# Performance work log

Measured on AMD Instinct MI355X. Metric: run time of the kernel, lower is better.

Reference implementation:

```python
import jax, jax.numpy as jnp
import numpy as np

K = 7  # g_decode_kernel_size


def _linear(x, W, b):
    # torch nn.Linear: y = x @ W.T + b, W: [out, in]
    return jnp.matmul(x, W.T) + b


def _shifted_conv(x, w, b):
    # x: [B, D, L]; causal conv: pad left K-1 (== pad both sides K-1 then trim right K-1)
    y = jax.lax.conv_general_dilated(
        x, w, window_strides=(1,), padding=[(K - 1, 0)],
        dimension_numbers=("NCH", "OIH", "NCH"))
    y = y + b[None, :, None]  # [B, 2D, L]
    D = x.shape[1]
    gated = y[:, :D, :] * jax.nn.sigmoid(y[:, D:, :])
    return gated + x


def setup_inputs() -> dict:
    key = jax.random.key(0)
    ks = jax.random.split(key, 16)
    B, T, L = 64, 64, 32
    E_enc, emb, D, A, V = 1024, 512, 512, 512, 30000

    def rn(k, shape, fan_in):
        return jax.random.normal(k, shape, dtype=jnp.float32) * (1.0 / np.sqrt(fan_in))

    return {
        "features": jax.random.normal(ks[0], (B, T, E_enc), dtype=jnp.float32),
        "captions": jax.random.randint(ks[1], (B, L), 0, V),
        "lengths": jax.random.randint(ks[2], (B,), 0, L),
        "embed_W": jax.random.normal(ks[3], (V, emb), dtype=jnp.float32) * 0.02,
        "W1": rn(ks[4], (D, emb + E_enc), emb + E_enc),
        "b1": jnp.zeros((D,), jnp.float32),
        "conv_w1": rn(ks[5], (2 * D, D, K), D * K),
        "conv_b1": jnp.zeros((2 * D,), jnp.float32),
        "conv_w2": rn(ks[6], (2 * D, D, K), D * K),
        "conv_b2": jnp.zeros((2 * D,), jnp.float32),
        "Wenc": rn(ks[7], (A, E_enc), E_enc),
        "benc": jnp.zeros((A,), jnp.float32),
        "Wdec": rn(ks[8], (A, D), D),
        "bdec": jnp.zeros((A,), jnp.float32),
        "Wp": rn(ks[9], (1, A), A),
        "bp": jnp.zeros((1,), jnp.float32),
        "W2": rn(ks[10], (V, E_enc + D), E_enc + D),
        "b2": jnp.zeros((V,), jnp.float32),
    }


def reference(features, captions, lengths, embed_W, W1, b1, conv_w1, conv_b1,
              conv_w2, conv_b2, Wenc, benc, Wdec, bdec, Wp, bp, W2, b2):
    # features: [B, T, E_enc]; captions: [B, L] int
    embeddings = embed_W[captions]                      # [B, L, emb]
    enc_mean = jnp.mean(features, axis=1, keepdims=True)  # [B, 1, E_enc]
    enc_mean = jnp.broadcast_to(enc_mean, (features.shape[0], embeddings.shape[1], features.shape[2]))
    x = jnp.concatenate([enc_mean, embeddings], axis=2)  # [B, L, E_enc+emb]
    x = _linear(x, W1, b1)                               # [B, L, D]
    x = jnp.transpose(x, (0, 2, 1))                      # [B, D, L]
    x = _shifted_conv(x, conv_w1, conv_b1)
    x = _shifted_conv(x, conv_w2, conv_b2)
    decode = jnp.transpose(x, (0, 2, 1))[:, :-1, :]      # [B, L-1, D]

    # Attention (vectorized over decode steps). NOTE: original code computes
    # tanh but discards it (assigns to misspelled 'featrues'), so NO tanh here.
    f_att = _linear(features, Wenc, benc)                # [B, T, A]
    d_att = _linear(decode, Wdec, bdec)                  # [B, S, A]
    # linear_prob applied to (f_att[:,None,t]+d_att[:,s,None]) -> scalar scores
    scores = (f_att[:, None, :, :] + d_att[:, :, None, :]) @ Wp[0] + bp[0]  # [B, S, T]
    attw = jax.nn.softmax(scores, axis=-1)               # softmax over T
    ctx = jnp.einsum("bst,bte->bse", attw, features)     # [B, S, E_enc]

    out = jnp.concatenate([ctx, decode], axis=2)         # [B, S, E_enc+D]
    logits = _linear(out, W2, b2)                        # [B, S, vocab]
    return logits
```

## Files before the change

### kernel.cpp

```cpp
#include <hip/hip_runtime.h>
#include <hip/hip_bf16.h>
#include <math.h>

#define B 64
#define T 64
#define E_ENC 1024
#define EMB 512
#define D 512
#define L 32
#define S 31
#define A 512
#define V 30000
#define KSZ 7
#define KC (D * KSZ)

typedef __attribute__((ext_vector_type(8))) short bf16x8;
typedef __attribute__((ext_vector_type(4))) float f32x4;

__device__ __forceinline__ unsigned short f2bf(float f) {
  union { float f; unsigned int u; } x; x.f = f;
  unsigned int r = (x.u + 0x7fffu + ((x.u >> 16) & 1u)) >> 16;
  return (unsigned short)r;
}

__device__ __forceinline__ void gload_lds16(const void* g, void* l) {
  __builtin_amdgcn_global_load_lds(
      (const __attribute__((address_space(1))) unsigned int*)g,
      (__attribute__((address_space(3))) unsigned int*)l, 16, 0, 0);
}

__global__ void k_wv(const float* __restrict__ Wenc, const float* __restrict__ Wp,
                     const float* __restrict__ benc, float* __restrict__ wv,
                     float* __restrict__ c0) {
  __shared__ float red[256];
  int e = blockIdx.x * 256 + threadIdx.x;
  float s = 0.f;
  for (int a = 0; a < A; ++a) s += Wp[a] * Wenc[(size_t)a * E_ENC + e];
  wv[e] = s;
  if (blockIdx.x == 0) {
    int t = threadIdx.x;
    float v = Wp[t] * benc[t] + Wp[t + 256] * benc[t + 256];
    red[t] = v;
    __syncthreads();
    for (int off = 128; off > 0; off >>= 1) {
      if (t < off) red[t] += red[t + off];
      __syncthreads();
    }
    if (t == 0) c0[0] = red[0];
  }
}

__global__ void k_mean_ctx(const float* __restrict__ features, const float* __restrict__ wv,
                           const float* __restrict__ c0, unsigned short* __restrict__ enc_meanb,
                           unsigned short* __restrict__ ctxb) {
  int b = blockIdx.x, tid = threadIdx.x;
  const float* fb = features + (size_t)b * T * E_ENC;
  __shared__ float s_attw[T];

  float m0 = 0, m1 = 0, m2 = 0, m3 = 0;
  for (int t = 0; t < T; ++t) {
    const float* r = fb + t * E_ENC;
    m0 += r[tid]; m1 += r[tid + 256]; m2 += r[tid + 512]; m3 += r[tid + 768];
  }
  size_t eb = (size_t)b * E_ENC;
  enc_meanb[eb + tid]       = f2bf(m0 * (1.f / 64.f));
  enc_meanb[eb + tid + 256] = f2bf(m1 * (1.f / 64.f));
  enc_meanb[eb + tid + 512] = f2bf(m2 * (1.f / 64.f));
  enc_meanb[eb + tid + 768] = f2bf(m3 * (1.f / 64.f));

  {
    int t = tid >> 2, part = tid & 3;
    const float* r = fb + t * E_ENC + part * 256;
    const float* wp = wv + part * 256;
    float s = 0.f;
    for (int e = 0; e < 256; e += 4) {
      float4 f4 = *(const float4*)(r + e);
      float4 w4 = *(const float4*)(wp + e);
      s += f4.x * w4.x + f4.y * w4.y + f4.z * w4.z + f4.w * w4.w;
    }
    s += __shfl_xor(s, 1);
    s += __shfl_xor(s, 2);
    if (part == 0) s_attw[t] = s + c0[0];
  }
  __syncthreads();
  if (tid < 64) {
    float v = s_attw[tid];
    float mx = v;
    #pragma unroll
    for (int off = 32; off > 0; off >>= 1) mx = fmaxf(mx, __shfl_xor(mx, off));
    float e = expf(v - mx);
    float sm = e;
    #pragma unroll
    for (int off = 32; off > 0; off >>= 1) sm += __shfl_xor(sm, off);
    s_attw[tid] = e / sm;
  }
  __syncthreads();
  float ca = 0, cb = 0, cc = 0, cd = 0;
  for (int t = 0; t < T; ++t) {
    float w = s_attw[t];
    const float* r = fb + t * E_ENC;
    ca += w * r[tid]; cb += w * r[tid + 256]; cc += w * r[tid + 512]; cd += w * r[tid + 768];
  }
  ctxb[eb + tid]       = f2bf(ca);
  ctxb[eb + tid + 256] = f2bf(cb);
  ctxb[eb + tid + 512] = f2bf(cc);
  ctxb[eb + tid + 768] = f2bf(cd);
}

__global__ void k_gather_emb(const float* __restrict__ embed_W,
                             const int* __restrict__ captions,
                             unsigned short* __restrict__ Xe) {
  int g = blockIdx.x, tid = threadIdx.x;
  int cap = captions[g];
  const float* src = embed_W + (size_t)cap * EMB;
  float2 v = *(const float2*)(src + tid * 2);
  unsigned int pk = (unsigned int)f2bf(v.x) | ((unsigned int)f2bf(v.y) << 16);
  *(unsigned int*)(Xe + (size_t)g * EMB + tid * 2) = pk;
}

__global__ void k_cvt_w1(const float* __restrict__ W1, unsigned short* __restrict__ w1b) {
  int d = blockIdx.x, tid = threadIdx.x;
  #pragma unroll
  for (int i = 0; i < 3; ++i) {
    int c = tid * 2 + i * 512;
    float2 v = *(const float2*)(W1 + (size_t)d * (E_ENC + EMB) + c);
    unsigned int pk = (unsigned int)f2bf(v.x) | ((unsigned int)f2bf(v.y) << 16);
    *(unsigned int*)(w1b + (size_t)d * (E_ENC + EMB) + c) = pk;
  }
}

__global__ __launch_bounds__(256) void k_x1f_mfma(
    const unsigned short* __restrict__ enc_meanb,
    const unsigned short* __restrict__ Xe,
    const unsigned short* __restrict__ w1b,
    const float* __restrict__ b1, float* __restrict__ x1) {
  __shared__ __align__(16) unsigned short As[64 * 64];
  __shared__ __align__(16) unsigned short Bs[64 * 64];
  int c0 = blockIdx.x * 64, g0 = blockIdx.y * 64;
  int tid = threadIdx.x, lane = tid & 63, wave = tid >> 6;
  int wr = wave >> 1, wc = wave & 1;
  int rsel = lane & 15, hi = lane >> 4;

  f32x4 acc[2][2];
  #pragma unroll
  for (int m = 0; m < 2; ++m)
    #pragma unroll
    for (int n = 0; n < 2; ++n) acc[m][n] = (f32x4){0.f, 0.f, 0.f, 0.f};

  int r1 = tid >> 3, s1 = tid & 7;
  int sw = (s1 ^ (r1 & 7)) * 8;
  const unsigned short* emA1 = enc_meanb + (size_t)(g0 >> 5) * 1024 + sw;
  const unsigned short* emA2 = enc_meanb + (size_t)((g0 >> 5) + 1) * 1024 + sw;
  const unsigned short* xeA1 = Xe + (size_t)(g0 + r1) * 512 + sw;
  const unsigned short* xeA2 = Xe + (size_t)(g0 + r1 + 32) * 512 + sw;
  const unsigned short* gB1 = w1b + (size_t)(c0 + r1) * (E_ENC + EMB) + sw;
  const unsigned short* gB2 = w1b + (size_t)(c0 + r1 + 32) * (E_ENC + EMB) + sw;
  unsigned short* aD1 = As + wave * 512;
  unsigned short* aD2 = As + 2048 + wave * 512;
  unsigned short* bD1 = Bs + wave * 512;
  unsigned short* bD2 = Bs + 2048 + wave * 512;

  int slot0 = hi ^ (rsel & 7);
  int slot1 = (4 + hi) ^ (rsel & 7);

  for (int kt = 0; kt < 24; ++kt) {
    const unsigned short *pA1, *pA2;
    if (kt < 16) { pA1 = emA1 + kt * 64; pA2 = emA2 + kt * 64; }
    else         { pA1 = xeA1 + (kt - 16) * 64; pA2 = xeA2 + (kt - 16) * 64; }
    gload_lds16(pA1, aD1);
    gload_lds16(pA2, aD2);
    gload_lds16(gB1, bD1);
    gload_lds16(gB2, bD2);
    gB1 += 64; gB2 += 64;
    __syncthreads();

    bf16x8 af[2][2], bfr[2][2];
    #pragma unroll
    for (int m = 0; m < 2; ++m) {
      int rowA = (wr * 32 + m * 16 + rsel) * 64;
      af[m][0] = *(const bf16x8*)(As + rowA + slot0 * 8);
      af[m][1] = *(const bf16x8*)(As + rowA + slot1 * 8);
    }
    #pragma unroll
    for (int n = 0; n < 2; ++n) {
      int rowB = (wc * 32 + n * 16 + rsel) * 64;
      bfr[n][0] = *(const bf16x8*)(Bs + rowB + slot0 * 8);
      bfr[n][1] = *(const bf16x8*)(Bs + rowB + slot1 * 8);
    }
    #pragma unroll
    for (int m = 0; m < 2; ++m)
      #pragma unroll
      for (int n = 0; n < 2; ++n) {
        acc[m][n] = __builtin_amdgcn_mfma_f32_16x16x32_bf16(af[m][0], bfr[n][0], acc[m][n], 0, 0, 0);
        acc[m][n] = __builtin_amdgcn_mfma_f32_16x16x32_bf16(af[m][1], bfr[n][1], acc[m][n], 0, 0, 0);
      }
    __syncthreads();
  }

  float bvv[2];
  #pragma unroll
  for (int n = 0; n < 2; ++n) bvv[n] = b1[c0 + wc * 32 + n * 16 + rsel];
  #pragma unroll
  for (int m = 0; m < 2; ++m)
    #pragma unroll
    for (int i = 0; i < 4; ++i) {
      int g = g0 + wr * 32 + m * 16 + hi * 4 + i;
      float* xr = x1 + (size_t)g * D;
      #pragma unroll
      for (int n = 0; n < 2; ++n) {
        int c = c0 + wc * 32 + n * 16 + rsel;
        xr[c] = acc[m][n][i] + bvv[n];
      }
    }
}

__global__ void k_im2col(const float* __restrict__ x, unsigned short* __restrict__ Xc) {
  int g = blockIdx.x, tid = threadIdx.x;
  int b = g >> 5, l = g & 31;
  unsigned short* row = Xc + (size_t)g * KC;
  const float* xb = x + (size_t)b * L * D;
  int d = tid * 2;
  #pragma unroll
  for (int k = 0; k < KSZ; ++k) {
    int lp = l + k - 6;
    unsigned int pk = 0;
    if (lp >= 0) {
      float2 v = *(const float2*)(xb + (size_t)lp * D + d);
      pk = (unsigned int)f2bf(v.x) | ((unsigned int)f2bf(v.y) << 16);
    }
    *(unsigned int*)(row + k * 512 + d) = pk;
  }
}

__global__ void k_cvt_wconv(const float* __restrict__ w, unsigned short* __restrict__ wb) {
  __shared__ float row[KC];
  int c = blockIdx.x, tid = threadIdx.x;
  const float* wr = w + (size_t)c * KC;
  for (int i = tid; i < KC; i += 256) row[i] = wr[i];
  __syncthreads();
  unsigned short* ob = wb + (size_t)c * KC;
  int dp = tid * 2;
  #pragma unroll
  for (int k = 0; k < KSZ; ++k) {
    unsigned int pk = (unsigned int)f2bf(row[dp * 7 + k]) |
                      ((unsigned int)f2bf(row[(dp + 1) * 7 + k]) << 16);
    *(unsigned int*)(ob + k * 512 + dp) = pk;
  }
}

template <int OUT_BF16>
__global__ __launch_bounds__(256) void k_conv_glu(
    const unsigned short* __restrict__ Xc, const unsigned short* __restrict__ wb,
    const float* __restrict__ bias, const float* __restrict__ xres,
    float* __restrict__ outf, unsigned short* __restrict__ outh) {
  __shared__ __align__(16) unsigned char csmem[32768];
  unsigned short (*As)[64 * 64] = (unsigned short (*)[64 * 64])csmem;
  unsigned short (*Bs)[64 * 64] = (unsigned short (*)[64 * 64])(csmem + 16384);
  int c0 = blockIdx.x * 32, g0 = blockIdx.y * 64;
  int tid = threadIdx.x, lane = tid & 63, wave = tid >> 6;
  int wr = wave >> 1, wc = wave & 1;
  int rsel = lane & 15, hi = lane >> 4;

  f32x4 acc[2][2];
  #pragma unroll
  for (int m = 0; m < 2; ++m)
    #pragma unroll
    for (int n = 0; n < 2; ++n) acc[m][n] = (f32x4){0.f, 0.f, 0.f, 0.f};

  int r1 = tid >> 3, s1 = tid & 7;
  int sw = (s1 ^ (r1 & 7)) * 8;
  const unsigned short* gA1 = Xc + (size_t)(g0 + r1) * KC + sw;
  const unsigned short* gA2 = Xc + (size_t)(g0 + r1 + 32) * KC + sw;
  const unsigned short* gB1 = wb + (size_t)(c0 + r1) * KC + sw;
  const unsigned short* gB2 = wb + (size_t)(512 + c0 + r1) * KC + sw;

  int slot0 = hi ^ (rsel & 7);
  int slot1 = (4 + hi) ^ (rsel & 7);

  gload_lds16(gA1, &As[0][wave * 512]);
  gload_lds16(gA2, &As[0][2048 + wave * 512]);
  gload_lds16(gB1, &Bs[0][wave * 512]);
  gload_lds16(gB2, &Bs[0][2048 + wave * 512]);
  gA1 += 64; gA2 += 64; gB1 += 64; gB2 += 64;
  __syncthreads();

  int cur = 0;
  for (int kt = 0; kt < KC / 64; ++kt) {
    if (kt + 1 < KC / 64) {
      int nb = cur ^ 1;
      gload_lds16(gA1, &As[nb][wave * 512]);
      gload_lds16(gA2, &As[nb][2048 + wave * 512]);
      gload_lds16(gB1, &Bs[nb][wave * 512]);
      gload_lds16(gB2, &Bs[nb][2048 + wave * 512]);
      gA1 += 64; gA2 += 64; gB1 += 64; gB2 += 64;
    }

    bf16x8 af[2][2], bfr[2][2];
    #pragma unroll
    for (int m = 0; m < 2; ++m) {
      int rowA = (wr * 32 + m * 16 + rsel) * 64;
      af[m][0] = *(const bf16x8*)(&As[cur][rowA + slot0 * 8]);
      af[m][1] = *(const bf16x8*)(&As[cur][rowA + slot1 * 8]);
    }
    #pragma unroll
    for (int n = 0; n < 2; ++n) {
      int rowB = (wc * 32 + n * 16 + rsel) * 64;
      bfr[n][0] = *(const bf16x8*)(&Bs[cur][rowB + slot0 * 8]);
      bfr[n][1] = *(const bf16x8*)(&Bs[cur][rowB + slot1 * 8]);
    }
    #pragma unroll
    for (int m = 0; m < 2; ++m)
      #pragma unroll
      for (int n = 0; n < 2; ++n) {
        acc[m][n] = __builtin_amdgcn_mfma_f32_16x16x32_bf16(af[m][0], bfr[n][0], acc[m][n], 0, 0, 0);
        acc[m][n] = __builtin_amdgcn_mfma_f32_16x16x32_bf16(af[m][1], bfr[n][1], acc[m][n], 0, 0, 0);
      }
    __syncthreads();
    cur ^= 1;
  }

  float* sb = (float*)csmem;
  float bvv[2];
  #pragma unroll
  for (int n = 0; n < 2; ++n)
    bvv[n] = wc ? bias[512 + c0 + n * 16 + rsel] : bias[c0 + n * 16 + rsel];
  if (wc) {
    #pragma unroll
    for (int m = 0; m < 2; ++m)
      #pragma unroll
      for (int i = 0; i < 4; ++i) {
        int lr = wr * 32 + m * 16 + hi * 4 + i;
        #pragma unroll
        for (int n = 0; n < 2; ++n)
          sb[lr * 33 + n * 16 + rsel] = acc[m][n][i] + bvv[n];
      }
  }
  __syncthreads();
  if (!wc) {
    #pragma unroll
    for (int m = 0; m < 2; ++m)
      #pragma unroll
      for (int i = 0; i < 4; ++i) {
        int lr = wr * 32 + m * 16 + hi * 4 + i;
        int g = g0 + lr;
        const float* xr = xres + (size_t)g * 512 + c0;
        #pragma unroll
        for (int n = 0; n < 2; ++n) {
          int d = n * 16 + rsel;
          float ya = acc[m][n][i] + bvv[n];
          float yb = sb[lr * 33 + d];
          float val = ya / (1.f + expf(-yb)) + xr[d];
          if (OUT_BF16) outh[(size_t)g * 512 + c0 + d] = f2bf(val);
          else          outf[(size_t)g * 512 + c0 + d] = val;
        }
      }
  }
}

__global__ __launch_bounds__(256) void k_cbase_mfma(
    const unsigned short* __restrict__ ctxb,
    const float* __restrict__ W2,
    const float* __restrict__ b2, float* __restrict__ cbase) {
  __shared__ __align__(16) unsigned short As[64 * 64];
  __shared__ __align__(16) unsigned short Bs[128 * 64];
  int v0 = blockIdx.x * 128;
  int tid = threadIdx.x, lane = tid & 63, wave = tid >> 6;
  int rsel = lane & 15, hi = lane >> 4;
  int wc = wave;

  f32x4 acc[4][2];
  #pragma unroll
  for (int m = 0; m < 4; ++m)
    #pragma unroll
    for (int n = 0; n < 2; ++n) acc[m][n] = (f32x4){0.f, 0.f, 0.f, 0.f};

  int ra1 = tid >> 3, sa = tid & 7;
  int ra2 = ra1 + 32;
  const unsigned short* gA1 = ctxb + (size_t)ra1 * 1024 + (sa ^ (ra1 & 7)) * 8;
  const unsigned short* gA2 = ctxb + (size_t)ra2 * 1024 + (sa ^ (ra2 & 7)) * 8;
  unsigned short* aD1 = As + wave * 512;
  unsigned short* aD2 = As + 2048 + wave * 512;

  const float* gB[4];
  int bofs[4];
  #pragma unroll
  for (int p = 0; p < 4; ++p) {
    int row = p * 32 + (tid >> 3);
    int seg = tid & 7;
    int vr = v0 + row; if (vr > V - 1) vr = V - 1;
    gB[p] = W2 + (size_t)vr * (E_ENC + D) + seg * 8;
    bofs[p] = row * 64 + (seg ^ (row & 7)) * 8;
  }

  for (int kt = 0; kt < 16; ++kt) {
    gload_lds16(gA1, aD1);
    gload_lds16(gA2, aD2);
    gA1 += 64; gA2 += 64;
    #pragma unroll
    for (int p = 0; p < 4; ++p) {
      float4 f0 = *(const float4*)(gB[p]);
      float4 f1 = *(const float4*)(gB[p] + 4);
      gB[p] += 64;
      bf16x8 o;
      o[0] = (short)f2bf(f0.x); o[1] = (short)f2bf(f0.y);
      o[2] = (short)f2bf(f0.z); o[3] = (short)f2bf(f0.w);
      o[4] = (short)f2bf(f1.x); o[5] = (short)f2bf(f1.y);
      o[6] = (short)f2bf(f1.z); o[7] = (short)f2bf(f1.w);
      *(bf16x8*)(Bs + bofs[p]) = o;
    }
    __syncthreads();

    bf16x8 af[4][2], bfr[2][2];
    #pragma unroll
    for (int m = 0; m < 4; ++m) {
      int rowA = (m * 16 + rsel) * 64;
      #pragma unroll
      for (int kk = 0; kk < 2; ++kk)
        af[m][kk] = *(const bf16x8*)(As + rowA + ((kk * 4 + hi) ^ (rsel & 7)) * 8);
    }
    #pragma unroll
    for (int n = 0; n < 2; ++n) {
      int rowB = (wc * 32 + n * 16 + rsel) * 64;
      #pragma unroll
      for (int kk = 0; kk < 2; ++kk)
        bfr[n][kk] = *(const bf16x8*)(Bs + rowB + ((kk * 4 + hi) ^ (rsel & 7)) * 8);
    }
    #pragma unroll
    for (int kk = 0; kk < 2; ++kk)
      #pragma unroll
      for (int m = 0; m < 4; ++m)
        #pragma unroll
        for (int n = 0; n < 2; ++n)
          acc[m][n] = __builtin_amdgcn_mfma_f32_16x16x32_bf16(af[m][kk], bfr[n][kk], acc[m][n], 0, 0, 0);
    __syncthreads();
  }

  #pragma unroll
  for (int n = 0; n < 2; ++n) {
    int v = v0 + wc * 32 + n * 16 + rsel;
    if (v >= V) continue;
    float bias = b2[v];
    #pragma unroll
    for (int m = 0; m < 4; ++m)
      #pragma unroll
      for (int i = 0; i < 4; ++i) {
        int b = m * 16 + hi * 4 + i;
        cbase[(size_t)b * V + v] = acc[m][n][i] + bias;
      }
  }
}

__global__ void k_cvt_w2d(const float* __restrict__ W2, unsigned short* __restrict__ y) {
  int i = blockIdx.x * 256 + threadIdx.x;
  int row = i >> 7, c = (i & 127) << 2;
  float4 f = *(const float4*)(W2 + (size_t)row * (E_ENC + D) + E_ENC + c);
  ushort4 o;
  o.x = f2bf(f.x); o.y = f2bf(f.y); o.z = f2bf(f.z); o.w = f2bf(f.w);
  *(ushort4*)(y + (size_t)row * D + c) = o;
}

__global__ __launch_bounds__(256) void k_logits_mfma(
    const unsigned short* __restrict__ Ab,
    const unsigned short* __restrict__ Bb,
    const float* __restrict__ cbase, float* __restrict__ out) {
  __shared__ __align__(16) unsigned char smem[33792];
  unsigned short (*As)[128 * 32] = (unsigned short (*)[128 * 32])smem;
  unsigned short (*Bs)[128 * 32] = (unsigned short (*)[128 * 32])(smem + 16384);
  int flat = blockIdx.x;
  int ord = (flat & 7) * 470 + (flat >> 3);
  int v0 = (ord >> 4) * 128, g0 = (ord & 15) * 128;
  int tid = threadIdx.x, lane = tid & 63, wave = tid >> 6;
  int wr = wave >> 1, wc = wave & 1;
  int rsel = lane & 15, hi = lane >> 4;

  f32x4 acc[4][4];
  #pragma unroll
  for (int m = 0; m < 4; ++m)
    #pragma unroll
    for (int n = 0; n < 4; ++n) acc[m][n] = (f32x4){0.f, 0.f, 0.f, 0.f};

  int r1 = tid >> 2, s1 = tid & 3;
  int seg = (s1 ^ ((r1 >> 1) & 3)) * 8;
  const unsigned short* gA1 = Ab + (size_t)(g0 + r1) * 512 + seg;
  const unsigned short* gA2 = Ab + (size_t)(g0 + r1 + 64) * 512 + seg;
  int vr1 = v0 + r1;      if (vr1 > V - 1) vr1 = V - 1;
  int vr2 = v0 + r1 + 64; if (vr2 > V - 1) vr2 = V - 1;
  const unsigned short* gB1 = Bb + (size_t)vr1 * 512 + seg;
  const unsigned short* gB2 = Bb + (size_t)vr2 * 512 + seg;

  gload_lds16(gA1, &As[0][wave * 512]);
  gload_lds16(gA2, &As[0][2048 + wave * 512]);
  gload_lds16(gB1, &Bs[0][wave * 512]);
  gload_lds16(gB2, &Bs[0][2048 + wave * 512]);
  gA1 += 32; gA2 += 32; gB1 += 32; gB2 += 32;
  __syncthreads();

  int sl = (rsel >> 1) & 3;
  int cur = 0;
  for (int kt = 0; kt < 16; ++kt) {
    if (kt + 1 < 16) {
      int nb = cur ^ 1;
      gload_lds16(gA1, &As[nb][wave * 512]);
      gload_lds16(gA2, &As[nb][2048 + wave * 512]);
      gload_lds16(gB1, &Bs[nb][wave * 512]);
      gload_lds16(gB2, &Bs[nb][2048 + wave * 512]);
      gA1 += 32; gA2 += 32; gB1 += 32; gB2 += 32;
    }

    bf16x8 af[4], bfr[4];
    #pragma unroll
    for (int m = 0; m < 4; ++m)
      af[m] = *(const bf16x8*)(&As[cur][(wr * 64 + m * 16 + rsel) * 32 + ((hi ^ sl) * 8)]);
    #pragma unroll
    for (int n = 0; n < 4; ++n)
      bfr[n] = *(const bf16x8*)(&Bs[cur][(wc * 64 + n * 16 + rsel) * 32 + ((hi ^ sl) * 8)]);
    #pragma unroll
    for (int m = 0; m < 4; ++m)
      #pragma unroll
      for (int n = 0; n < 4; ++n)
        acc[m][n] = __builtin_amdgcn_mfma_f32_16x16x32_bf16(af[m], bfr[n], acc[m][n], 0, 0, 0);
    __syncthreads();
    cur ^= 1;
  }

  float* ebuf = (float*)smem;
  #pragma unroll
  for (int h = 0; h < 2; ++h) {
    if (h) __syncthreads();
    if (wr == h) {
      #pragma unroll
      for (int m = 0; m < 4; ++m)
        #pragma unroll
        for (int i = 0; i < 4; ++i) {
          int lr = m * 16 + hi * 4 + i;
          #pragma unroll
          for (int n = 0; n < 4; ++n)
            ebuf[lr * 132 + wc * 64 + n * 16 + rsel] = acc[m][n][i];
        }
    }
    __syncthreads();
    #pragma unroll
    for (int j = 0; j < 8; ++j) {
      int f = tid + j * 256;
      int lr = f >> 5, c4 = (f & 31) * 4;
      int g = g0 + h * 64 + lr;
      int b = g >> 5, lt = g & 31;
      int v = v0 + c4;
      if (lt < S && v < V) {
        float4 val = *(const float4*)(ebuf + lr * 132 + c4);
        float4 cb4 = *(const float4*)(cbase + (size_t)b * V + v);
        float4 o;
        o.x = val.x + cb4.x; o.y = val.y + cb4.y;
        o.z = val.z + cb4.z; o.w = val.w + cb4.w;
        *(float4*)(out + ((size_t)b * S + lt) * V + v) = o;
      }
    }
  }
}

extern "C" void kernel_launch(void* const* d_in, const int* in_sizes, int n_in,
                              void* d_out, int out_size, void* d_ws, size_t ws_size,
                              hipStream_t stream) {
  const float* features = (const float*)d_in[0];
  const int*   captions = (const int*)d_in[1];
  const float* embed_W  = (const float*)d_in[3];
  const float* W1   = (const float*)d_in[4];
  const float* b1   = (const float*)d_in[5];
  const float* cw1  = (const float*)d_in[6];
  const float* cb1  = (const float*)d_in[7];
  const float* cw2  = (const float*)d_in[8];
  const float* cb2  = (const float*)d_in[9];
  const float* Wenc = (const float*)d_in[10];
  const float* benc = (const float*)d_in[11];
  const float* Wp   = (const float*)d_in[14];
  const float* W2   = (const float*)d_in[16];
  const float* b2   = (const float*)d_in[17];
  float* out = (float*)d_out;

  float* ws = (float*)d_ws;
  float* wv       = ws;
  float* c0       = ws + 1024;
  unsigned short* enc_meanb = (unsigned short*)(ws + 1040);
  unsigned short* ctxb = (unsigned short*)(ws + 66576);
  float* xA       = ws + 164880;
  float* xB       = ws + 1213456;
  float* cbase    = ws + 2262032;
  unsigned short* x3b  = (unsigned short*)xA;
  unsigned short* Xc   = (unsigned short*)(ws + 4359184);
  unsigned short* wbuf = (unsigned short*)(ws + 8029200);
  unsigned short* W2d  = (unsigned short*)(ws + 9864208);
  unsigned short* Xe  = Xc;
  unsigned short* w1b = Xc + 1048576;

  hipLaunchKernelGGL(k_cvt_w2d,  dim3(15000),   dim3(256), 0, stream, W2, W2d);
  hipLaunchKernelGGL(k_wv,       dim3(4),       dim3(256), 0, stream, Wenc, Wp, benc, wv, c0);
  hipLaunchKernelGGL(k_mean_ctx, dim3(B),       dim3(256), 0, stream, features, wv, c0, enc_meanb, ctxb);

  hipLaunchKernelGGL(k_gather_emb, dim3(2048),  dim3(256), 0, stream, embed_W, captions, Xe);
  hipLaunchKernelGGL(k_cvt_w1,     dim3(512),   dim3(256), 0, stream, W1, w1b);
  hipLaunchKernelGGL(k_x1f_mfma,   dim3(8, 32), dim3(256), 0, stream, enc_meanb, Xe, w1b, b1, xA);

  hipLaunchKernelGGL(k_cvt_wconv,   dim3(1024),   dim3(256), 0, stream, cw1, wbuf);
  hipLaunchKernelGGL(k_im2col,      dim3(2048),   dim3(256), 0, stream, xA, Xc);
  hipLaunchKernelGGL(k_conv_glu<0>, dim3(16, 32), dim3(256), 0, stream, Xc, wbuf, cb1, xA, xB, (unsigned short*)nullptr);

  hipLaunchKernelGGL(k_cvt_wconv,   dim3(1024),   dim3(256), 0, stream, cw2, wbuf);
  hipLaunchKernelGGL(k_im2col,      dim3(2048),   dim3(256), 0, stream, xB, Xc);
  hipLaunchKernelGGL(k_conv_glu<1>, dim3(16, 32), dim3(256), 0, stream, Xc, wbuf, cb2, xB, (float*)nullptr, x3b);

  hipLaunchKernelGGL(k_cbase_mfma, dim3(235),   dim3(256), 0, stream, ctxb, W2, b2, cbase);
  hipLaunchKernelGGL(k_logits_mfma, dim3(3760), dim3(256), 0, stream, x3b, W2d, cbase, out);
}
```

Before: 370.5 us.

## Triple-buffer logits GEMM LDS pipeline and split k_wv reduction across waves

The logits MFMA kernel moves from a double-buffered LDS scheme to a three-stage ring. Two k-tiles are prefetched ahead, and explicit vmcnt waits with raw s_barriers replace __syncthreads. This should hide more global-load latency behind MFMA work, at the cost of 48KB LDS per block, which may reduce occupancy. Separately, k_wv now splits the 512-long reduction over four waves with an LDS combine and launches 16 blocks instead of 4, to raise parallelism in that small kernel.

```diff
diff --git a/kernel.cpp b/kernel.cpp
--- a/kernel.cpp
+++ b/kernel.cpp
@@ -32,11 +32,16 @@
 __global__ void k_wv(const float* __restrict__ Wenc, const float* __restrict__ Wp,
                      const float* __restrict__ benc, float* __restrict__ wv,
                      float* __restrict__ c0) {
+  __shared__ float sp[4][64];
   __shared__ float red[256];
-  int e = blockIdx.x * 256 + threadIdx.x;
+  int el = threadIdx.x & 63, part = threadIdx.x >> 6;
+  int e = blockIdx.x * 64 + el;
   float s = 0.f;
-  for (int a = 0; a < A; ++a) s += Wp[a] * Wenc[(size_t)a * E_ENC + e];
-  wv[e] = s;
+  for (int a = part * 128; a < part * 128 + 128; ++a)
+    s += Wp[a] * Wenc[(size_t)a * E_ENC + e];
+  sp[part][el] = s;
+  __syncthreads();
+  if (part == 0) wv[e] = sp[0][el] + sp[1][el] + sp[2][el] + sp[3][el];
   if (blockIdx.x == 0) {
     int t = threadIdx.x;
     float v = Wp[t] * benc[t] + Wp[t + 256] * benc[t + 256];
@@ -463,9 +468,7 @@
     const unsigned short* __restrict__ Ab,
     const unsigned short* __restrict__ Bb,
     const float* __restrict__ cbase, float* __restrict__ out) {
-  __shared__ __align__(16) unsigned char smem[33792];
-  unsigned short (*As)[128 * 32] = (unsigned short (*)[128 * 32])smem;
-  unsigned short (*Bs)[128 * 32] = (unsigned short (*)[128 * 32])(smem + 16384);
+  __shared__ __align__(16) unsigned char smem[49152];
   int flat = blockIdx.x;
   int ord = (flat & 7) * 470 + (flat >> 3);
   int v0 = (ord >> 4) * 128, g0 = (ord & 15) * 128;
@@ -488,40 +491,55 @@
   const unsigned short* gB1 = Bb + (size_t)vr1 * 512 + seg;
   const unsigned short* gB2 = Bb + (size_t)vr2 * 512 + seg;
 
-  gload_lds16(gA1, &As[0][wave * 512]);
-  gload_lds16(gA2, &As[0][2048 + wave * 512]);
-  gload_lds16(gB1, &Bs[0][wave * 512]);
-  gload_lds16(gB2, &Bs[0][2048 + wave * 512]);
-  gA1 += 32; gA2 += 32; gB1 += 32; gB2 += 32;
-  __syncthreads();
+  int wofs = wave * 512;
+
+#define L_STAGE(bi)                                                        \
+  do {                                                                     \
+    unsigned short* aB = (unsigned short*)(smem + (bi) * 8192);            \
+    unsigned short* bB = (unsigned short*)(smem + 24576 + (bi) * 8192);    \
+    gload_lds16(gA1, aB + wofs);                                           \
+    gload_lds16(gA2, aB + 2048 + wofs);                                    \
+    gload_lds16(gB1, bB + wofs);                                           \
+    gload_lds16(gB2, bB + 2048 + wofs);                                    \
+    gA1 += 32; gA2 += 32; gB1 += 32; gB2 += 32;                            \
+  } while (0)
+
+  L_STAGE(0);
+  L_STAGE(1);
 
   int sl = (rsel >> 1) & 3;
-  int cur = 0;
+  int sidx = 2, cidx = 0;
   for (int kt = 0; kt < 16; ++kt) {
-    if (kt + 1 < 16) {
-      int nb = cur ^ 1;
-      gload_lds16(gA1, &As[nb][wave * 512]);
-      gload_lds16(gA2, &As[nb][2048 + wave * 512]);
-      gload_lds16(gB1, &Bs[nb][wave * 512]);
-      gload_lds16(gB2, &Bs[nb][2048 + wave * 512]);
-      gA1 += 32; gA2 += 32; gB1 += 32; gB2 += 32;
-    }
-
+    if (kt < 14) L_STAGE(sidx);
+    __builtin_amdgcn_sched_barrier(0);
+    if (kt < 14)       asm volatile("s_waitcnt vmcnt(8)" ::: "memory");
+    else if (kt == 14) asm volatile("s_waitcnt vmcnt(4)" ::: "memory");
+    else               asm volatile("s_waitcnt vmcnt(0)" ::: "memory");
+    __builtin_amdgcn_sched_barrier(0);
+    __builtin_amdgcn_s_barrier();
+    __builtin_amdgcn_sched_barrier(0);
+
+    const unsigned short* Ac = (const unsigned short*)(smem + cidx * 8192);
+    const unsigned short* Bc = (const unsigned short*)(smem + 24576 + cidx * 8192);
     bf16x8 af[4], bfr[4];
     #pragma unroll
     for (int m = 0; m < 4; ++m)
-      af[m] = *(const bf16x8*)(&As[cur][(wr * 64 + m * 16 + rsel) * 32 + ((hi ^ sl) * 8)]);
+      af[m] = *(const bf16x8*)(Ac + (wr * 64 + m * 16 + rsel) * 32 + ((hi ^ sl) * 8));
     #pragma unroll
     for (int n = 0; n < 4; ++n)
-      bfr[n] = *(const bf16x8*)(&Bs[cur][(wc * 64 + n * 16 + rsel) * 32 + ((hi ^ sl) * 8)]);
+      bfr[n] = *(const bf16x8*)(Bc + (wc * 64 + n * 16 + rsel) * 32 + ((hi ^ sl) * 8));
     #pragma unroll
     for (int m = 0; m < 4; ++m)
       #pragma unroll
       for (int n = 0; n < 4; ++n)
         acc[m][n] = __builtin_amdgcn_mfma_f32_16x16x32_bf16(af[m], bfr[n], acc[m][n], 0, 0, 0);
-    __syncthreads();
-    cur ^= 1;
-  }
+
+    __builtin_amdgcn_sched_barrier(0);
+    __builtin_amdgcn_s_barrier();
+    sidx = cidx;
+    cidx = (cidx + 1 == 3) ? 0 : cidx + 1;
+  }
+#undef L_STAGE
 
   float* ebuf = (float*)smem;
   #pragma unroll
@@ -593,7 +611,7 @@
   unsigned short* w1b = Xc + 1048576;
 
   hipLaunchKernelGGL(k_cvt_w2d,  dim3(15000),   dim3(256), 0, stream, W2, W2d);
-  hipLaunchKernelGGL(k_wv,       dim3(4),       dim3(256), 0, stream, Wenc, Wp, benc, wv, c0);
+  hipLaunchKernelGGL(k_wv,       dim3(16),      dim3(256), 0, stream, Wenc, Wp, benc, wv, c0);
   hipLaunchKernelGGL(k_mean_ctx, dim3(B),       dim3(256), 0, stream, features, wv, c0, enc_meanb, ctxb);
 
   hipLaunchKernelGGL(k_gather_emb, dim3(2048),  dim3(256), 0, stream, embed_W, captions, Xe);
```

Result: no change. 368.3 us (-0.6%).
